# Kernel tuning notes

Measured on AMD Instinct MI355X. Metric: run time of the kernel, lower is better.

Reference implementation:

```python
import jax, jax.numpy as jnp
import numpy as np

B = 4096      # number of snakes (graphs)
L = 256       # fixed snake length (nodes per chain)
N = B * L     # total nodes
HID = 32
OUT = 32
AUX = 32
FIN = 64
N_FRUITS = 1
AUX_IN = 2 + 1 + N_FRUITS * 2  # = 5


def _chain_edges():
    # chain edges i<->i+1 within each graph, both directions (PyG undirected chain)
    base = np.arange(L - 1)
    src1 = (np.arange(B)[:, None] * L + base[None, :]).ravel()
    dst1 = src1 + 1
    src = np.concatenate([src1, dst1])
    dst = np.concatenate([dst1, src1])
    return np.stack([src, dst]).astype(np.int64)  # [2, 2*(L-1)*B]


def setup_inputs() -> dict:
    key = jax.random.key(0)
    ks = jax.random.split(key, 16)

    def lin(k, fan_in, fan_out):
        k1, k2 = jax.random.split(k)
        bound = 1.0 / np.sqrt(fan_in)
        W = jax.random.uniform(k1, (fan_in, fan_out), jnp.float32, -bound, bound)
        b = jax.random.uniform(k2, (fan_out,), jnp.float32, -bound, bound)
        return W, b

    x = jax.random.normal(ks[0], (N, 2), jnp.float32)
    heads = jax.random.normal(ks[1], (B, 2), jnp.float32)
    body_sizes = jax.random.uniform(ks[2], (B, 1), jnp.float32)
    fruits = jax.random.normal(ks[3], (B, N_FRUITS, 2), jnp.float32)

    W1, b1 = lin(ks[4], 2, HID)
    W2, b2 = lin(ks[5], HID, HID)
    Wr, br = lin(ks[6], HID, OUT)
    Wa1, ba1 = lin(ks[7], AUX_IN, AUX)
    Wa2, ba2 = lin(ks[8], AUX, AUX)
    Wc, bc = lin(ks[9], OUT + AUX, FIN)
    Wp, bp = lin(ks[10], FIN, 5)
    Wv, bv = lin(ks[11], FIN, 1)

    edge_index = jnp.asarray(_chain_edges())
    batch_ids = jnp.repeat(jnp.arange(B, dtype=jnp.int64), L)

    return dict(x=x, heads=heads, body_sizes=body_sizes, fruits=fruits,
                W1=W1, b1=b1, W2=W2, b2=b2, Wr=Wr, br=br,
                Wa1=Wa1, ba1=ba1, Wa2=Wa2, ba2=ba2, Wc=Wc, bc=bc,
                Wp=Wp, bp=bp, Wv=Wv, bv=bv,
                edge_index=edge_index, batch_ids=batch_ids)


def _gcn_conv(h, W, b, src, dst):
    # PyG GCNConv: out = D^{-1/2} (A + I) D^{-1/2} (h W) + b, deg counts self-loop
    h = h @ W  # [N, F]
    ones = jnp.ones(src.shape[0], h.dtype)
    deg = jax.ops.segment_sum(ones, dst, num_segments=N) + 1.0  # self-loop
    dinv = jax.lax.rsqrt(deg)
    norm = dinv[src] * dinv[dst]  # [E]
    agg = jax.ops.segment_sum(norm[:, None] * h[src], dst, num_segments=N)
    agg = agg + (dinv * dinv)[:, None] * h  # self-loop messages
    return agg + b


def reference(x, heads, body_sizes, fruits,
              W1, b1, W2, b2, Wr, br, Wa1, ba1, Wa2, ba2,
              Wc, bc, Wp, bp, Wv, bv, edge_index, batch_ids):
    src, dst = edge_index[0], edge_index[1]
    h = jax.nn.relu(_gcn_conv(x, W1, b1, src, dst))
    h = jax.nn.relu(_gcn_conv(h, W2, b2, src, dst))
    # global mean pool per graph
    pooled = jax.ops.segment_sum(h, batch_ids, num_segments=B)
    counts = jax.ops.segment_sum(jnp.ones(N, h.dtype), batch_ids, num_segments=B)
    pooled = pooled / counts[:, None]
    body_emb = pooled @ Wr + br  # [B, OUT]

    aux_input = jnp.concatenate([heads, body_sizes,
                                 fruits.reshape(fruits.shape[0], -1)], axis=-1)
    aux = jax.nn.relu(aux_input @ Wa1 + ba1)
    aux = jax.nn.relu(aux @ Wa2 + ba2)

    combined = jnp.concatenate([body_emb, aux], axis=-1)
    combined = jax.nn.relu(combined @ Wc + bc)
    logits = combined @ Wp + bp  # [B, 5]
    value = combined @ Wv + bv   # [B, 1]
    return logits, value
```

## Files before the change

kernel.cpp:

```cpp
#include <hip/hip_runtime.h>
#include <hip/hip_bf16.h>


#define NB  4096
#define CL  256
#define HID 32
#define FIN 64
#define SPB 4

typedef __attribute__((ext_vector_type(8))) short    bf16x8;
typedef __attribute__((ext_vector_type(4))) float    f32x4;
typedef __attribute__((ext_vector_type(4))) unsigned u32x4;

__device__ __forceinline__ unsigned pkbf(float a, float b) {
    __hip_bfloat162 hb = __float22bfloat162_rn(make_float2(a, b));
    unsigned u; __builtin_memcpy(&u, &hb, sizeof(u));
    return u;
}
__device__ __forceinline__ float bflo(unsigned u) { return __builtin_bit_cast(float, u << 16); }
__device__ __forceinline__ float bfhi(unsigned u) { return __builtin_bit_cast(float, u & 0xffff0000u); }

__device__ __forceinline__ void gcn_coef(int n, float& nc, float& nl, float& nr) {
    const float IS3 = 0.57735026918962576f, IS2 = 0.70710678118654752f;
    const float dn = (n == 0 || n == CL - 1) ? IS2 : IS3;
    nc = dn * dn;
    nl = (n > 0)      ? dn * ((n == 1)      ? IS2 : IS3) : 0.0f;
    nr = (n < CL - 1) ? dn * ((n == CL - 2) ? IS2 : IS3) : 0.0f;
}

__global__ __launch_bounds__(256, 4) void snake_fused(
    const float* __restrict__ x,
    const float* __restrict__ heads,
    const float* __restrict__ body_sizes,
    const float* __restrict__ fruits,
    const float* __restrict__ W1, const float* __restrict__ b1,
    const float* __restrict__ W2, const float* __restrict__ b2,
    const float* __restrict__ Wr, const float* __restrict__ br,
    const float* __restrict__ Wa1, const float* __restrict__ ba1,
    const float* __restrict__ Wa2, const float* __restrict__ ba2,
    const float* __restrict__ Wc, const float* __restrict__ bc,
    const float* __restrict__ Wp, const float* __restrict__ bp,
    const float* __restrict__ Wv, const float* __restrict__ bv,
    float* __restrict__ out)
{
    __shared__ __align__(16) float edgebuf[SPB][4][2][HID];
    __shared__ __align__(16) float waveparts[SPB][HID][4];
    __shared__ __align__(16) float poolLDS[SPB][HID];
    __shared__ __align__(16) float auxLDS[SPB][HID];
    __shared__ __align__(16) float catLDS[SPB][FIN];

    const int blk  = blockIdx.x;
    const int i    = threadIdx.x;
    const int w    = i >> 6;
    const int lane = i & 63;
    const int g    = lane >> 4;
    const int c    = lane & 15;

    bf16x8 Bh[2], Bl[2];
    #pragma unroll
    for (int nt = 0; nt < 2; ++nt) {
        unsigned hh[4], ll[4];
        #pragma unroll
        for (int p = 0; p < 4; ++p) {
            const float wa = W2[(8 * g + 2 * p)     * HID + c + 16 * nt];
            const float wb = W2[(8 * g + 2 * p + 1) * HID + c + 16 * nt];
            const unsigned hu = pkbf(wa, wb);
            hh[p] = hu;
            ll[p] = pkbf(wa - bflo(hu), wb - bfhi(hu));
        }
        u32x4 H = {hh[0], hh[1], hh[2], hh[3]};
        u32x4 L = {ll[0], ll[1], ll[2], ll[3]};
        Bh[nt] = __builtin_bit_cast(bf16x8, H);
        Bl[nt] = __builtin_bit_cast(bf16x8, L);
    }
    const float b2v0 = b2[c], b2v1 = b2[c + 16];

    const float4 W1a0 = *reinterpret_cast<const float4*>(W1 + 8 * g);
    const float4 W1a1 = *reinterpret_cast<const float4*>(W1 + 8 * g + 4);
    const float4 W1b0 = *reinterpret_cast<const float4*>(W1 + HID + 8 * g);
    const float4 W1b1 = *reinterpret_cast<const float4*>(W1 + HID + 8 * g + 4);
    const float4 b1v0 = *reinterpret_cast<const float4*>(b1 + 8 * g);
    const float4 b1v1 = *reinterpret_cast<const float4*>(b1 + 8 * g + 4);

    float ncd, nld, nrd;
    gcn_coef(i, ncd, nld, nrd);

    const float THIRD = 0.33333333333333333f;
    const float I23   = 0.40824829046386302f;
    const bool fixL = (w == 0) && (g == 0);
    const bool fixR = (w == 3) && (g == 3);

    #pragma unroll 1
    for (int s = 0; s < SPB; ++s) {
        const int gs = SPB * blk + s;
        const float2* xs = reinterpret_cast<const float2*>(x) + gs * CL;

        const float2 xc = xs[i];
        const float2 xl = xs[i - (i > 0)];
        const float2 xr = xs[i + (i < CL - 1)];
        const float sxx = ncd * xc.x + nld * xl.x + nrd * xr.x;
        const float sxy = ncd * xc.y + nld * xl.y + nrd * xr.y;

        float sxA[4], syA[4];
        #pragma unroll
        for (int t = 0; t < 4; ++t) {
            sxA[t] = __shfl(sxx, 16 * t + c, 64);
            syA[t] = __shfl(sxy, 16 * t + c, 64);
        }

        f32x4 acc[4][2];
        #pragma unroll
        for (int t = 0; t < 4; ++t)
            #pragma unroll
            for (int nt = 0; nt < 2; ++nt) { f32x4 z = {0.f, 0.f, 0.f, 0.f}; acc[t][nt] = z; }

        #pragma unroll
        for (int t = 0; t < 4; ++t) {
            const float sa = sxA[t], sb = syA[t];
            const float r0 = fmaxf(fmaf(sa, W1a0.x, fmaf(sb, W1b0.x, b1v0.x)), 0.f);
            const float r1 = fmaxf(fmaf(sa, W1a0.y, fmaf(sb, W1b0.y, b1v0.y)), 0.f);
            const float r2 = fmaxf(fmaf(sa, W1a0.z, fmaf(sb, W1b0.z, b1v0.z)), 0.f);
            const float r3 = fmaxf(fmaf(sa, W1a0.w, fmaf(sb, W1b0.w, b1v0.w)), 0.f);
            const float r4 = fmaxf(fmaf(sa, W1a1.x, fmaf(sb, W1b1.x, b1v1.x)), 0.f);
            const float r5 = fmaxf(fmaf(sa, W1a1.y, fmaf(sb, W1b1.y, b1v1.y)), 0.f);
            const float r6 = fmaxf(fmaf(sa, W1a1.z, fmaf(sb, W1b1.z, b1v1.z)), 0.f);
            const float r7 = fmaxf(fmaf(sa, W1a1.w, fmaf(sb, W1b1.w, b1v1.w)), 0.f);
            const unsigned h0 = pkbf(r0, r1), h1 = pkbf(r2, r3);
            const unsigned h2 = pkbf(r4, r5), h3 = pkbf(r6, r7);
            const unsigned q0 = pkbf(r0 - bflo(h0), r1 - bfhi(h0));
            const unsigned q1 = pkbf(r2 - bflo(h1), r3 - bfhi(h1));
            const unsigned q2 = pkbf(r4 - bflo(h2), r5 - bfhi(h2));
            const unsigned q3 = pkbf(r6 - bflo(h3), r7 - bfhi(h3));
            u32x4 HU = {h0, h1, h2, h3};
            u32x4 LU = {q0, q1, q2, q3};
            const bf16x8 ah = __builtin_bit_cast(bf16x8, HU);
            const bf16x8 al = __builtin_bit_cast(bf16x8, LU);
            #pragma unroll
            for (int nt = 0; nt < 2; ++nt) {
                acc[t][nt] = __builtin_amdgcn_mfma_f32_16x16x32_bf16(ah, Bh[nt], acc[t][nt], 0, 0, 0);
                acc[t][nt] = __builtin_amdgcn_mfma_f32_16x16x32_bf16(al, Bh[nt], acc[t][nt], 0, 0, 0);
                acc[t][nt] = __builtin_amdgcn_mfma_f32_16x16x32_bf16(ah, Bl[nt], acc[t][nt], 0, 0, 0);
            }
        }

        if (lane < 16) {
            edgebuf[s][w][0][c]      = acc[0][0][0];
            edgebuf[s][w][0][c + 16] = acc[0][1][0];
        } else if (lane >= 48) {
            edgebuf[s][w][1][c]      = acc[3][0][3];
            edgebuf[s][w][1][c + 16] = acc[3][1][3];
        }
        __syncthreads();

        float sum0 = 0.f, sum1 = 0.f;
        #pragma unroll
        for (int t = 0; t < 4; ++t) {
            float c0 = THIRD, r0c = THIRD, l1c = THIRD;
            float c3 = THIRD, l3c = THIRD, r2c = THIRD;
            if (t == 0) { c0 = fixL ? 0.5f : THIRD; r0c = fixL ? I23 : THIRD; l1c = fixL ? I23 : THIRD; }
            if (t == 3) { c3 = fixR ? 0.5f : THIRD; l3c = fixR ? I23 : THIRD; r2c = fixR ? I23 : THIRD; }
            #pragma unroll
            for (int nt = 0; nt < 2; ++nt) {
                const f32x4 v = acc[t][nt];
                const float Lsend = (g == 3) ? acc[(t > 0) ? t - 1 : 0][nt][3] : acc[t][nt][3];
                const int   Lsrc  = (g == 0) ? (c + 48) : (lane - 16);
                float L = __shfl(Lsend, Lsrc, 64);
                if (t == 0) {
                    float eL = edgebuf[s][(w > 0) ? w - 1 : 0][1][c + 16 * nt];
                    eL = (w > 0) ? eL : 0.f;
                    L = (g == 0) ? eL : L;
                }
                const float Rsend = (g == 0) ? acc[(t < 3) ? t + 1 : 3][nt][0] : acc[t][nt][0];
                const int   Rsrc  = (g == 3) ? c : (lane + 16);
                float R = __shfl(Rsend, Rsrc, 64);
                if (t == 3) {
                    float eR = edgebuf[s][(w < 3) ? w + 1 : 3][0][c + 16 * nt];
                    eR = (w < 3) ? eR : 0.f;
                    R = (g == 3) ? eR : R;
                }
                const float bb = (nt == 0) ? b2v0 : b2v1;
                const float h0 = fmaxf(fmaf(c0,    v[0], fmaf(THIRD, L,    fmaf(r0c,  v[1], bb))), 0.f);
                const float h1 = fmaxf(fmaf(THIRD, v[1], fmaf(l1c,   v[0], fmaf(THIRD, v[2], bb))), 0.f);
                const float h2 = fmaxf(fmaf(THIRD, v[2], fmaf(THIRD, v[1], fmaf(r2c,  v[3], bb))), 0.f);
                const float h3 = fmaxf(fmaf(c3,    v[3], fmaf(l3c,   v[2], fmaf(THIRD, R,   bb))), 0.f);
                const float hs = (h0 + h1) + (h2 + h3);
                if (nt == 0) sum0 += hs; else sum1 += hs;
            }
        }
        sum0 += __shfl_xor(sum0, 16, 64); sum0 += __shfl_xor(sum0, 32, 64);
        sum1 += __shfl_xor(sum1, 16, 64); sum1 += __shfl_xor(sum1, 32, 64);
        if (g == 0) {
            waveparts[s][c][w]      = sum0;
            waveparts[s][c + 16][w] = sum1;
        }
    }
    __syncthreads();

    const int gsH = SPB * blk + w;
    if (lane < HID) {
        const f32x4 wp = *reinterpret_cast<const f32x4*>(&waveparts[w][lane][0]);
        poolLDS[w][lane] = (wp.x + wp.y + wp.z + wp.w) * (1.0f / CL);
    } else {
        const int cc = lane - HID;
        float a = ba1[cc];
        a = fmaf(heads[2 * gsH],      Wa1[0 * HID + cc], a);
        a = fmaf(heads[2 * gsH + 1],  Wa1[1 * HID + cc], a);
        a = fmaf(body_sizes[gsH],     Wa1[2 * HID + cc], a);
        a = fmaf(fruits[2 * gsH],     Wa1[3 * HID + cc], a);
        a = fmaf(fruits[2 * gsH + 1], Wa1[4 * HID + cc], a);
        auxLDS[w][cc] = fmaxf(a, 0.f);
    }
    __syncthreads();

    if (lane < HID) {
        float be0 = br[lane], be1 = 0.f;
        const float4* p4 = reinterpret_cast<const float4*>(poolLDS[w]);
        #pragma unroll
        for (int k4 = 0; k4 < 8; ++k4) {
            const float4 p = p4[k4];
            be0 = fmaf(p.x, Wr[(4 * k4 + 0) * HID + lane], be0);
            be1 = fmaf(p.y, Wr[(4 * k4 + 1) * HID + lane], be1);
            be0 = fmaf(p.z, Wr[(4 * k4 + 2) * HID + lane], be0);
            be1 = fmaf(p.w, Wr[(4 * k4 + 3) * HID + lane], be1);
        }
        catLDS[w][lane] = be0 + be1;
    } else {
        const int cc = lane - HID;
        float a0 = ba2[cc], a1 = 0.f;
        const float4* p4 = reinterpret_cast<const float4*>(auxLDS[w]);
        #pragma unroll
        for (int k4 = 0; k4 < 8; ++k4) {
            const float4 p = p4[k4];
            a0 = fmaf(p.x, Wa2[(4 * k4 + 0) * HID + cc], a0);
            a1 = fmaf(p.y, Wa2[(4 * k4 + 1) * HID + cc], a1);
            a0 = fmaf(p.z, Wa2[(4 * k4 + 2) * HID + cc], a0);
            a1 = fmaf(p.w, Wa2[(4 * k4 + 3) * HID + cc], a1);
        }
        catLDS[w][lane] = fmaxf(a0 + a1, 0.f);
    }
    __syncthreads();

    {
        float cb0 = bc[lane], cb1 = 0.f;
        const float4* c4p = reinterpret_cast<const float4*>(catLDS[w]);
        #pragma unroll
        for (int k4 = 0; k4 < 16; ++k4) {
            const float4 p = c4p[k4];
            cb0 = fmaf(p.x, Wc[(4 * k4 + 0) * FIN + lane], cb0);
            cb1 = fmaf(p.y, Wc[(4 * k4 + 1) * FIN + lane], cb1);
            cb0 = fmaf(p.z, Wc[(4 * k4 + 2) * FIN + lane], cb0);
            cb1 = fmaf(p.w, Wc[(4 * k4 + 3) * FIN + lane], cb1);
        }
        const float cb = fmaxf(cb0 + cb1, 0.f);
        float s0 = cb * Wp[lane * 5 + 0];
        float s1 = cb * Wp[lane * 5 + 1];
        float s2 = cb * Wp[lane * 5 + 2];
        float s3 = cb * Wp[lane * 5 + 3];
        float s4 = cb * Wp[lane * 5 + 4];
        float s5 = cb * Wv[lane];
        #pragma unroll
        for (int m = 1; m <= 32; m <<= 1) {
            s0 += __shfl_xor(s0, m, 64);
            s1 += __shfl_xor(s1, m, 64);
            s2 += __shfl_xor(s2, m, 64);
            s3 += __shfl_xor(s3, m, 64);
            s4 += __shfl_xor(s4, m, 64);
            s5 += __shfl_xor(s5, m, 64);
        }
        if (lane == 0) {
            out[gsH * 5 + 0] = s0 + bp[0];
            out[gsH * 5 + 1] = s1 + bp[1];
            out[gsH * 5 + 2] = s2 + bp[2];
            out[gsH * 5 + 3] = s3 + bp[3];
            out[gsH * 5 + 4] = s4 + bp[4];
            out[NB * 5 + gsH] = s5 + bv[0];
        }
    }
}

extern "C" void kernel_launch(void* const* d_in, const int* in_sizes, int n_in,
                              void* d_out, int out_size, void* d_ws, size_t ws_size,
                              hipStream_t stream) {
    const float* x          = (const float*)d_in[0];
    const float* heads      = (const float*)d_in[1];
    const float* body_sizes = (const float*)d_in[2];
    const float* fruits     = (const float*)d_in[3];
    const float* W1 = (const float*)d_in[4];
    const float* b1 = (const float*)d_in[5];
    const float* W2 = (const float*)d_in[6];
    const float* b2 = (const float*)d_in[7];
    const float* Wr = (const float*)d_in[8];
    const float* br = (const float*)d_in[9];
    const float* Wa1 = (const float*)d_in[10];
    const float* ba1 = (const float*)d_in[11];
    const float* Wa2 = (const float*)d_in[12];
    const float* ba2 = (const float*)d_in[13];
    const float* Wc = (const float*)d_in[14];
    const float* bc = (const float*)d_in[15];
    const float* Wp = (const float*)d_in[16];
    const float* bp = (const float*)d_in[17];
    const float* Wv = (const float*)d_in[18];
    const float* bv = (const float*)d_in[19];

    float* out = (float*)d_out;
    snake_fused<<<NB / SPB, CL, 0, stream>>>(
        x, heads, body_sizes, fruits,
        W1, b1, W2, b2, Wr, br, Wa1, ba1, Wa2, ba2,
        Wc, bc, Wp, bp, Wv, bv, out);
}
```

Baseline: 126.8 us.

## Assign one snake per wave, removing block barriers and LDS edge exchange

```diff
diff --git a/kernel.cpp b/kernel.cpp
--- a/kernel.cpp
+++ b/kernel.cpp
@@ -26,6 +26,12 @@
     nc = dn * dn;
     nl = (n > 0)      ? dn * ((n == 1)      ? IS2 : IS3) : 0.0f;
     nr = (n < CL - 1) ? dn * ((n == CL - 2) ? IS2 : IS3) : 0.0f;
+}
+
+__device__ __forceinline__ void wave_lds_fence() {
+    __builtin_amdgcn_wave_barrier();
+    asm volatile("s_waitcnt lgkmcnt(0)" ::: "memory");
+    __builtin_amdgcn_wave_barrier();
 }
 
 __global__ __launch_bounds__(256, 4) void snake_fused(
@@ -43,18 +49,16 @@
     const float* __restrict__ Wv, const float* __restrict__ bv,
     float* __restrict__ out)
 {
-    __shared__ __align__(16) float edgebuf[SPB][4][2][HID];
-    __shared__ __align__(16) float waveparts[SPB][HID][4];
     __shared__ __align__(16) float poolLDS[SPB][HID];
     __shared__ __align__(16) float auxLDS[SPB][HID];
     __shared__ __align__(16) float catLDS[SPB][FIN];
 
     const int blk  = blockIdx.x;
-    const int i    = threadIdx.x;
-    const int w    = i >> 6;
-    const int lane = i & 63;
+    const int w    = threadIdx.x >> 6;
+    const int lane = threadIdx.x & 63;
     const int g    = lane >> 4;
     const int c    = lane & 15;
+    const int gs   = SPB * blk + w;
 
     bf16x8 Bh[2], Bl[2];
     #pragma unroll
@@ -82,77 +86,78 @@
     const float4 b1v0 = *reinterpret_cast<const float4*>(b1 + 8 * g);
     const float4 b1v1 = *reinterpret_cast<const float4*>(b1 + 8 * g + 4);
 
-    float ncd, nld, nrd;
-    gcn_coef(i, ncd, nld, nrd);
+    const float2* xs = reinterpret_cast<const float2*>(x) + gs * CL;
+
+    float sxx[4], sxy[4];
+    {
+        float2 xc4[4], xl4[4], xr4[4];
+        #pragma unroll
+        for (int k = 0; k < 4; ++k) {
+            const int n = 64 * k + lane;
+            xc4[k] = xs[n];
+            xl4[k] = xs[n - (n > 0)];
+            xr4[k] = xs[n + (n < CL - 1)];
+        }
+        #pragma unroll
+        for (int k = 0; k < 4; ++k) {
+            const int n = 64 * k + lane;
+            float ncd, nld, nrd;
+            gcn_coef(n, ncd, nld, nrd);
+            sxx[k] = ncd * xc4[k].x + nld * xl4[k].x + nrd * xr4[k].x;
+            sxy[k] = ncd * xc4[k].y + nld * xl4[k].y + nrd * xr4[k].y;
+        }
+    }
+
+    auto mfma_tile = [&](float sxk, float syk, int t, f32x4& d0, f32x4& d1) {
+        const float sa = __shfl(sxk, 16 * t + c, 64);
+        const float sb = __shfl(syk, 16 * t + c, 64);
+        const float r0 = fmaxf(fmaf(sa, W1a0.x, fmaf(sb, W1b0.x, b1v0.x)), 0.f);
+        const float r1 = fmaxf(fmaf(sa, W1a0.y, fmaf(sb, W1b0.y, b1v0.y)), 0.f);
+        const float r2 = fmaxf(fmaf(sa, W1a0.z, fmaf(sb, W1b0.z, b1v0.z)), 0.f);
+        const float r3 = fmaxf(fmaf(sa, W1a0.w, fmaf(sb, W1b0.w, b1v0.w)), 0.f);
+        const float r4 = fmaxf(fmaf(sa, W1a1.x, fmaf(sb, W1b1.x, b1v1.x)), 0.f);
+        const float r5 = fmaxf(fmaf(sa, W1a1.y, fmaf(sb, W1b1.y, b1v1.y)), 0.f);
+        const float r6 = fmaxf(fmaf(sa, W1a1.z, fmaf(sb, W1b1.z, b1v1.z)), 0.f);
+        const float r7 = fmaxf(fmaf(sa, W1a1.w, fmaf(sb, W1b1.w, b1v1.w)), 0.f);
+        const unsigned h0 = pkbf(r0, r1), h1 = pkbf(r2, r3);
+        const unsigned h2 = pkbf(r4, r5), h3 = pkbf(r6, r7);
+        const unsigned q0 = pkbf(r0 - bflo(h0), r1 - bfhi(h0));
+        const unsigned q1 = pkbf(r2 - bflo(h1), r3 - bfhi(h1));
+        const unsigned q2 = pkbf(r4 - bflo(h2), r5 - bfhi(h2));
+        const unsigned q3 = pkbf(r6 - bflo(h3), r7 - bfhi(h3));
+        u32x4 HU = {h0, h1, h2, h3};
+        u32x4 LU = {q0, q1, q2, q3};
+        const bf16x8 ah = __builtin_bit_cast(bf16x8, HU);
+        const bf16x8 al = __builtin_bit_cast(bf16x8, LU);
+        const f32x4 z = {0.f, 0.f, 0.f, 0.f};
+        d0 = __builtin_amdgcn_mfma_f32_16x16x32_bf16(ah, Bh[0], z,  0, 0, 0);
+        d0 = __builtin_amdgcn_mfma_f32_16x16x32_bf16(al, Bh[0], d0, 0, 0, 0);
+        d0 = __builtin_amdgcn_mfma_f32_16x16x32_bf16(ah, Bl[0], d0, 0, 0, 0);
+        d1 = __builtin_amdgcn_mfma_f32_16x16x32_bf16(ah, Bh[1], z,  0, 0, 0);
+        d1 = __builtin_amdgcn_mfma_f32_16x16x32_bf16(al, Bh[1], d1, 0, 0, 0);
+        d1 = __builtin_amdgcn_mfma_f32_16x16x32_bf16(ah, Bl[1], d1, 0, 0, 0);
+    };
+
+    f32x4 accCur[4][2];
+    f32x4 accN0[2];
+
+    #pragma unroll
+    for (int t = 0; t < 4; ++t)
+        mfma_tile(sxx[0], sxy[0], t, accCur[t][0], accCur[t][1]);
+
+    float edgeL0 = 0.f, edgeL1 = 0.f;
+    float sum0 = 0.f, sum1 = 0.f;
 
     const float THIRD = 0.33333333333333333f;
     const float I23   = 0.40824829046386302f;
-    const bool fixL = (w == 0) && (g == 0);
-    const bool fixR = (w == 3) && (g == 3);
-
-    #pragma unroll 1
-    for (int s = 0; s < SPB; ++s) {
-        const int gs = SPB * blk + s;
-        const float2* xs = reinterpret_cast<const float2*>(x) + gs * CL;
-
-        const float2 xc = xs[i];
-        const float2 xl = xs[i - (i > 0)];
-        const float2 xr = xs[i + (i < CL - 1)];
-        const float sxx = ncd * xc.x + nld * xl.x + nrd * xr.x;
-        const float sxy = ncd * xc.y + nld * xl.y + nrd * xr.y;
-
-        float sxA[4], syA[4];
-        #pragma unroll
-        for (int t = 0; t < 4; ++t) {
-            sxA[t] = __shfl(sxx, 16 * t + c, 64);
-            syA[t] = __shfl(sxy, 16 * t + c, 64);
-        }
-
-        f32x4 acc[4][2];
-        #pragma unroll
-        for (int t = 0; t < 4; ++t)
-            #pragma unroll
-            for (int nt = 0; nt < 2; ++nt) { f32x4 z = {0.f, 0.f, 0.f, 0.f}; acc[t][nt] = z; }
-
-        #pragma unroll
-        for (int t = 0; t < 4; ++t) {
-            const float sa = sxA[t], sb = syA[t];
-            const float r0 = fmaxf(fmaf(sa, W1a0.x, fmaf(sb, W1b0.x, b1v0.x)), 0.f);
-            const float r1 = fmaxf(fmaf(sa, W1a0.y, fmaf(sb, W1b0.y, b1v0.y)), 0.f);
-            const float r2 = fmaxf(fmaf(sa, W1a0.z, fmaf(sb, W1b0.z, b1v0.z)), 0.f);
-            const float r3 = fmaxf(fmaf(sa, W1a0.w, fmaf(sb, W1b0.w, b1v0.w)), 0.f);
-            const float r4 = fmaxf(fmaf(sa, W1a1.x, fmaf(sb, W1b1.x, b1v1.x)), 0.f);
-            const float r5 = fmaxf(fmaf(sa, W1a1.y, fmaf(sb, W1b1.y, b1v1.y)), 0.f);
-            const float r6 = fmaxf(fmaf(sa, W1a1.z, fmaf(sb, W1b1.z, b1v1.z)), 0.f);
-            const float r7 = fmaxf(fmaf(sa, W1a1.w, fmaf(sb, W1b1.w, b1v1.w)), 0.f);
-            const unsigned h0 = pkbf(r0, r1), h1 = pkbf(r2, r3);
-            const unsigned h2 = pkbf(r4, r5), h3 = pkbf(r6, r7);
-            const unsigned q0 = pkbf(r0 - bflo(h0), r1 - bfhi(h0));
-            const unsigned q1 = pkbf(r2 - bflo(h1), r3 - bfhi(h1));
-            const unsigned q2 = pkbf(r4 - bflo(h2), r5 - bfhi(h2));
-            const unsigned q3 = pkbf(r6 - bflo(h3), r7 - bfhi(h3));
-            u32x4 HU = {h0, h1, h2, h3};
-            u32x4 LU = {q0, q1, q2, q3};
-            const bf16x8 ah = __builtin_bit_cast(bf16x8, HU);
-            const bf16x8 al = __builtin_bit_cast(bf16x8, LU);
-            #pragma unroll
-            for (int nt = 0; nt < 2; ++nt) {
-                acc[t][nt] = __builtin_amdgcn_mfma_f32_16x16x32_bf16(ah, Bh[nt], acc[t][nt], 0, 0, 0);
-                acc[t][nt] = __builtin_amdgcn_mfma_f32_16x16x32_bf16(al, Bh[nt], acc[t][nt], 0, 0, 0);
-                acc[t][nt] = __builtin_amdgcn_mfma_f32_16x16x32_bf16(ah, Bl[nt], acc[t][nt], 0, 0, 0);
-            }
-        }
-
-        if (lane < 16) {
-            edgebuf[s][w][0][c]      = acc[0][0][0];
-            edgebuf[s][w][0][c + 16] = acc[0][1][0];
-        } else if (lane >= 48) {
-            edgebuf[s][w][1][c]      = acc[3][0][3];
-            edgebuf[s][w][1][c + 16] = acc[3][1][3];
-        }
-        __syncthreads();
-
-        float sum0 = 0.f, sum1 = 0.f;
+
+    #pragma unroll
+    for (int k = 0; k < 4; ++k) {
+        if (k < 3) mfma_tile(sxx[k + 1], sxy[k + 1], 0, accN0[0], accN0[1]);
+
+        const bool fixL = (k == 0) && (g == 0);
+        const bool fixR = (k == 3) && (g == 3);
+
         #pragma unroll
         for (int t = 0; t < 4; ++t) {
             float c0 = THIRD, r0c = THIRD, l1c = THIRD;
@@ -161,56 +166,61 @@
             if (t == 3) { c3 = fixR ? 0.5f : THIRD; l3c = fixR ? I23 : THIRD; r2c = fixR ? I23 : THIRD; }
             #pragma unroll
             for (int nt = 0; nt < 2; ++nt) {
-                const f32x4 v = acc[t][nt];
-                const float Lsend = (g == 3) ? acc[(t > 0) ? t - 1 : 0][nt][3] : acc[t][nt][3];
+                const f32x4 v = accCur[t][nt];
+                const float Lsend = (g == 3) ? accCur[(t > 0) ? t - 1 : 0][nt][3] : accCur[t][nt][3];
                 const int   Lsrc  = (g == 0) ? (c + 48) : (lane - 16);
                 float L = __shfl(Lsend, Lsrc, 64);
                 if (t == 0) {
-                    float eL = edgebuf[s][(w > 0) ? w - 1 : 0][1][c + 16 * nt];
-                    eL = (w > 0) ? eL : 0.f;
+                    float eL = __shfl((nt == 0) ? edgeL0 : edgeL1, 48 + c, 64);
+                    eL = (k > 0) ? eL : 0.f;
                     L = (g == 0) ? eL : L;
                 }
-                const float Rsend = (g == 0) ? acc[(t < 3) ? t + 1 : 3][nt][0] : acc[t][nt][0];
+                const float Rsend = (g == 0) ? accCur[(t < 3) ? t + 1 : 3][nt][0] : accCur[t][nt][0];
                 const int   Rsrc  = (g == 3) ? c : (lane + 16);
                 float R = __shfl(Rsend, Rsrc, 64);
                 if (t == 3) {
-                    float eR = edgebuf[s][(w < 3) ? w + 1 : 3][0][c + 16 * nt];
-                    eR = (w < 3) ? eR : 0.f;
+                    float eR = __shfl(accN0[nt][0], c, 64);
+                    eR = (k < 3) ? eR : 0.f;
                     R = (g == 3) ? eR : R;
                 }
                 const float bb = (nt == 0) ? b2v0 : b2v1;
-                const float h0 = fmaxf(fmaf(c0,    v[0], fmaf(THIRD, L,    fmaf(r0c,  v[1], bb))), 0.f);
+                const float h0 = fmaxf(fmaf(c0,    v[0], fmaf(THIRD, L,    fmaf(r0c,   v[1], bb))), 0.f);
                 const float h1 = fmaxf(fmaf(THIRD, v[1], fmaf(l1c,   v[0], fmaf(THIRD, v[2], bb))), 0.f);
-                const float h2 = fmaxf(fmaf(THIRD, v[2], fmaf(THIRD, v[1], fmaf(r2c,  v[3], bb))), 0.f);
-                const float h3 = fmaxf(fmaf(c3,    v[3], fmaf(l3c,   v[2], fmaf(THIRD, R,   bb))), 0.f);
+                const float h2 = fmaxf(fmaf(THIRD, v[2], fmaf(THIRD, v[1], fmaf(r2c,   v[3], bb))), 0.f);
+                const float h3 = fmaxf(fmaf(c3,    v[3], fmaf(l3c,   v[2], fmaf(THIRD, R,    bb))), 0.f);
                 const float hs = (h0 + h1) + (h2 + h3);
                 if (nt == 0) sum0 += hs; else sum1 += hs;
             }
         }
-        sum0 += __shfl_xor(sum0, 16, 64); sum0 += __shfl_xor(sum0, 32, 64);
-        sum1 += __shfl_xor(sum1, 16, 64); sum1 += __shfl_xor(sum1, 32, 64);
-        if (g == 0) {
-            waveparts[s][c][w]      = sum0;
-            waveparts[s][c + 16][w] = sum1;
-        }
-    }
-    __syncthreads();
-
-    const int gsH = SPB * blk + w;
-    if (lane < HID) {
-        const f32x4 wp = *reinterpret_cast<const f32x4*>(&waveparts[w][lane][0]);
-        poolLDS[w][lane] = (wp.x + wp.y + wp.z + wp.w) * (1.0f / CL);
-    } else {
+
+        edgeL0 = accCur[3][0][3];
+        edgeL1 = accCur[3][1][3];
+        if (k < 3) {
+            accCur[0][0] = accN0[0];
+            accCur[0][1] = accN0[1];
+            #pragma unroll
+            for (int t = 1; t < 4; ++t)
+                mfma_tile(sxx[k + 1], sxy[k + 1], t, accCur[t][0], accCur[t][1]);
+        }
+    }
+
+    sum0 += __shfl_xor(sum0, 16, 64); sum0 += __shfl_xor(sum0, 32, 64);
+    sum1 += __shfl_xor(sum1, 16, 64); sum1 += __shfl_xor(sum1, 32, 64);
+
+    if (lane < 16) {
+        poolLDS[w][lane]      = sum0 * (1.0f / CL);
+        poolLDS[w][lane + 16] = sum1 * (1.0f / CL);
+    } else if (lane >= HID) {
         const int cc = lane - HID;
         float a = ba1[cc];
-        a = fmaf(heads[2 * gsH],      Wa1[0 * HID + cc], a);
-        a = fmaf(heads[2 * gsH + 1],  Wa1[1 * HID + cc], a);
-        a = fmaf(body_sizes[gsH],     Wa1[2 * HID + cc], a);
-        a = fmaf(fruits[2 * gsH],     Wa1[3 * HID + cc], a);
-        a = fmaf(fruits[2 * gsH + 1], Wa1[4 * HID + cc], a);
+        a = fmaf(heads[2 * gs],      Wa1[0 * HID + cc], a);
+        a = fmaf(heads[2 * gs + 1],  Wa1[1 * HID + cc], a);
+        a = fmaf(body_sizes[gs],     Wa1[2 * HID + cc], a);
+        a = fmaf(fruits[2 * gs],     Wa1[3 * HID + cc], a);
+        a = fmaf(fruits[2 * gs + 1], Wa1[4 * HID + cc], a);
         auxLDS[w][cc] = fmaxf(a, 0.f);
     }
-    __syncthreads();
+    wave_lds_fence();
 
     if (lane < HID) {
         float be0 = br[lane], be1 = 0.f;
@@ -238,7 +248,7 @@
         }
         catLDS[w][lane] = fmaxf(a0 + a1, 0.f);
     }
-    __syncthreads();
+    wave_lds_fence();
 
     {
         float cb0 = bc[lane], cb1 = 0.f;
@@ -268,12 +278,12 @@
             s5 += __shfl_xor(s5, m, 64);
         }
         if (lane == 0) {
-            out[gsH * 5 + 0] = s0 + bp[0];
-            out[gsH * 5 + 1] = s1 + bp[1];
-            out[gsH * 5 + 2] = s2 + bp[2];
-            out[gsH * 5 + 3] = s3 + bp[3];
-            out[gsH * 5 + 4] = s4 + bp[4];
-            out[NB * 5 + gsH] = s5 + bv[0];
+            out[gs * 5 + 0] = s0 + bp[0];
+            out[gs * 5 + 1] = s1 + bp[1];
+            out[gs * 5 + 2] = s2 + bp[2];
+            out[gs * 5 + 3] = s3 + bp[3];
+            out[gs * 5 + 4] = s4 + bp[4];
+            out[NB * 5 + gs] = s5 + bv[0];
         }
     }
 }
```

Result: no change. 125.0 us (-1.4%).
